# Kernel optimization log

Measured on AMD Instinct MI355X. Metric: run time of the kernel, lower is better.

The kernel has to match this reference:

```python
import jax, jax.numpy as jnp
import numpy as np

LN_EPS = 1e-5


def setup_inputs() -> dict:
    key = jax.random.key(0)
    k1, k2, k3, k4 = jax.random.split(key, 4)
    b, n, d, o, m = 64, 196, 768, 196, 2
    return {
        "x": jax.random.normal(k1, (b, n, d), dtype=jnp.float32),
        "ln_w": jnp.ones((d,), dtype=jnp.float32),
        "ln_b": jnp.zeros((d,), dtype=jnp.float32),
        "sw": jax.random.normal(k2, (o, m, n), dtype=jnp.float32),
        "sb": jax.random.normal(k3, (o, m, n), dtype=jnp.float32),
        "dw": jax.random.normal(k4, (o, m), dtype=jnp.float32),
    }


def reference(x, ln_w, ln_b, sw, sb, dw):
    # LayerNorm over last dim (dim=768)
    mu = jnp.mean(x, axis=-1, keepdims=True)
    var = jnp.mean(jnp.square(x - mu), axis=-1, keepdims=True)
    y = (x - mu) * jax.lax.rsqrt(var + LN_EPS) * ln_w + ln_b  # (b, n, d)

    # Original: repeat y to (b,d,o,m,n), apply sw*y+sb, sum over n.
    # With no synapse activation / dropout this is exactly a contraction:
    # s[b,d,o,m] = sum_n sw[o,m,n]*y[b,n,d] + sum_n sb[o,m,n]
    s = jnp.einsum('bnd,omn->bdom', y, sw) + jnp.sum(sb, axis=-1)  # (b,d,o,m)

    # dendritic weighting then sum over branches m
    t = jnp.sum(dw * s, axis=-1)  # (b, d, o)

    # soma = nn.GELU (exact erf form)
    out = jax.nn.gelu(t, approximate=False)

    out = jnp.transpose(out, (0, 2, 1))  # (b, o, d) == (b, n, d)
    return x * (out + 1.0)
```

## Files before the change

kernel.cpp:

```cpp
#include <hip/hip_runtime.h>
#include <math.h>


#define B_   64
#define N_   196
#define D_   768
#define KP   256

typedef __attribute__((ext_vector_type(8))) short bf16x8;
typedef __attribute__((ext_vector_type(4))) float f32x4;

__device__ __forceinline__ unsigned short bf16_rne(float f) {
    unsigned u = __builtin_bit_cast(unsigned, f);
    u += 0x7FFFu + ((u >> 16) & 1u);
    return (unsigned short)(u >> 16);
}
__device__ __forceinline__ float bf16_to_f(unsigned short h) {
    unsigned u = ((unsigned)h) << 16;
    return __builtin_bit_cast(float, u);
}

__global__ void prep_w_kernel(const float* __restrict__ sw,
                              const float* __restrict__ sb,
                              const float* __restrict__ dw,
                              unsigned short* __restrict__ Whi,
                              unsigned short* __restrict__ Wlo,
                              float* __restrict__ rowsum,
                              float* __restrict__ cvec) {
    int o = blockIdx.x;
    int t = threadIdx.x;
    float w0 = 0.f, w1 = 0.f;
    if (o < N_) { w0 = dw[o * 2 + 0]; w1 = dw[o * 2 + 1]; }
    float val = 0.f, sbp = 0.f;
    if (o < N_ && t < N_) {
        val = w0 * sw[(o * 2 + 0) * N_ + t] + w1 * sw[(o * 2 + 1) * N_ + t];
        sbp = w0 * sb[(o * 2 + 0) * N_ + t] + w1 * sb[(o * 2 + 1) * N_ + t];
    }
    unsigned short h = bf16_rne(val);
    Whi[o * KP + t] = h;
    Wlo[o * KP + t] = bf16_rne(val - bf16_to_f(h));
    __shared__ float r1[256], r2[256];
    r1[t] = val; r2[t] = sbp;
    __syncthreads();
    for (int s = 128; s > 0; s >>= 1) {
        if (t < s) { r1[t] += r1[t + s]; r2[t] += r2[t + s]; }
        __syncthreads();
    }
    if (t == 0) { rowsum[o] = r1[0]; cvec[o] = r2[0]; }
}

__global__ void ln_stats_kernel(const float* __restrict__ x,
                                float* __restrict__ mu,
                                float* __restrict__ rstd) {
    int wave = threadIdx.x >> 6;
    int lane = threadIdx.x & 63;
    int row  = blockIdx.x * 4 + wave;
    const float4* xr = reinterpret_cast<const float4*>(x + (size_t)row * D_);
    float4 v0 = xr[lane];
    float4 v1 = xr[lane + 64];
    float4 v2 = xr[lane + 128];
    float s = v0.x + v0.y + v0.z + v0.w
            + v1.x + v1.y + v1.z + v1.w
            + v2.x + v2.y + v2.z + v2.w;
    #pragma unroll
    for (int off = 32; off >= 1; off >>= 1) s += __shfl_xor(s, off);
    float m = s * (1.0f / D_);
    float q = 0.f;
    {
        float d;
        d = v0.x - m; q += d * d;  d = v0.y - m; q += d * d;
        d = v0.z - m; q += d * d;  d = v0.w - m; q += d * d;
        d = v1.x - m; q += d * d;  d = v1.y - m; q += d * d;
        d = v1.z - m; q += d * d;  d = v1.w - m; q += d * d;
        d = v2.x - m; q += d * d;  d = v2.y - m; q += d * d;
        d = v2.z - m; q += d * d;  d = v2.w - m; q += d * d;
    }
    #pragma unroll
    for (int off = 32; off >= 1; off >>= 1) q += __shfl_xor(q, off);
    if (lane == 0) {
        mu[row]   = m;
        rstd[row] = rsqrtf(q * (1.0f / D_) + 1e-5f);
    }
}

__global__ __launch_bounds__(512, 4) void gemm_mfma_kernel(
    const float* __restrict__ x,
    const float* __restrict__ ln_w,
    const float* __restrict__ ln_b,
    const unsigned short* __restrict__ Whi,
    const unsigned short* __restrict__ Wlo,
    const float* __restrict__ rowsum,
    const float* __restrict__ cvec,
    const float* __restrict__ mu,
    const float* __restrict__ rstd,
    float* __restrict__ out) {
    const int b  = blockIdx.y;
    const int d0 = blockIdx.x * 64;
    const int t = threadIdx.x;
    const int w = t >> 6, lane = t & 63;
    const int m16 = lane & 15, g = lane >> 4;

    __shared__ __align__(16) unsigned short BsH[32 * 64 * 8];
    __shared__ __align__(16) unsigned short BsL[32 * 64 * 8];

    const float* xb  = x + (size_t)b * (N_ * D_);
    const float* mub = mu + b * N_;
    const float* rsb = rstd + b * N_;

    float xv[4][8];
    #pragma unroll
    for (int p = 0; p < 4; ++p) {
        const int koct = p * 8 + w;
        #pragma unroll
        for (int e = 0; e < 8; ++e) {
            const int k = koct * 8 + e;
            xv[p][e] = (k < N_) ? xb[(size_t)k * D_ + d0 + lane] : 0.f;
        }
    }
    #pragma unroll
    for (int p = 0; p < 4; ++p) {
        const int koct = p * 8 + w;
        bf16x8 hv, lv;
        #pragma unroll
        for (int e = 0; e < 8; ++e) {
            const int k = koct * 8 + e;
            float v = 0.f;
            if (k < N_) v = (xv[p][e] - mub[k]) * rsb[k];
            unsigned short h = bf16_rne(v);
            hv[e] = (short)h;
            lv[e] = (short)bf16_rne(v - bf16_to_f(h));
        }
        const int addr = (koct * 64 + lane) * 8;
        *reinterpret_cast<bf16x8*>(&BsH[addr]) = hv;
        *reinterpret_cast<bf16x8*>(&BsL[addr]) = lv;
    }
    __syncthreads();

    f32x4 acc[2][4];
    #pragma unroll
    for (int i = 0; i < 2; ++i)
        #pragma unroll
        for (int j = 0; j < 4; ++j)
            acc[i][j] = (f32x4){0.f, 0.f, 0.f, 0.f};

    const int arow0 = (w * 32 + 0 * 16 + m16) * KP;
    const int arow1 = (w * 32 + 1 * 16 + m16) * KP;

    bf16x8 ah[2][2], al[2][2];
    ah[0][0] = *reinterpret_cast<const bf16x8*>(&Whi[arow0 + g * 8]);
    ah[0][1] = *reinterpret_cast<const bf16x8*>(&Whi[arow1 + g * 8]);
    al[0][0] = *reinterpret_cast<const bf16x8*>(&Wlo[arow0 + g * 8]);
    al[0][1] = *reinterpret_cast<const bf16x8*>(&Wlo[arow1 + g * 8]);

    #pragma unroll
    for (int kq = 0; kq < 7; ++kq) {
        const int cur = kq & 1, nxt = cur ^ 1;
        if (kq < 6) {
            const int col = (kq + 1) * 32 + g * 8;
            ah[nxt][0] = *reinterpret_cast<const bf16x8*>(&Whi[arow0 + col]);
            ah[nxt][1] = *reinterpret_cast<const bf16x8*>(&Whi[arow1 + col]);
            al[nxt][0] = *reinterpret_cast<const bf16x8*>(&Wlo[arow0 + col]);
            al[nxt][1] = *reinterpret_cast<const bf16x8*>(&Wlo[arow1 + col]);
        }
        #pragma unroll
        for (int nf = 0; nf < 4; ++nf) {
            const int baddr = ((kq * 4 + g) * 64 + nf * 16 + m16) * 8;
            bf16x8 bh = *reinterpret_cast<const bf16x8*>(&BsH[baddr]);
            bf16x8 bl = *reinterpret_cast<const bf16x8*>(&BsL[baddr]);
            #pragma unroll
            for (int mf = 0; mf < 2; ++mf) {
                acc[mf][nf] = __builtin_amdgcn_mfma_f32_16x16x32_bf16(ah[cur][mf], bh, acc[mf][nf], 0, 0, 0);
                acc[mf][nf] = __builtin_amdgcn_mfma_f32_16x16x32_bf16(ah[cur][mf], bl, acc[mf][nf], 0, 0, 0);
                acc[mf][nf] = __builtin_amdgcn_mfma_f32_16x16x32_bf16(al[cur][mf], bh, acc[mf][nf], 0, 0, 0);
            }
        }
    }

    float lwv[4], lbv[4];
    #pragma unroll
    for (int nf = 0; nf < 4; ++nf) {
        lwv[nf] = ln_w[d0 + nf * 16 + m16];
        lbv[nf] = ln_b[d0 + nf * 16 + m16];
    }
    #pragma unroll
    for (int mf = 0; mf < 2; ++mf) {
        #pragma unroll
        for (int r = 0; r < 4; ++r) {
            const int o = w * 32 + mf * 16 + g * 4 + r;
            if (o < N_) {
                const float rs = rowsum[o], cc = cvec[o];
                #pragma unroll
                for (int nf = 0; nf < 4; ++nf) {
                    const int d = d0 + nf * 16 + m16;
                    float T = fmaf(lwv[nf], acc[mf][nf][r], fmaf(lbv[nf], rs, cc));
                    float gl = 0.5f * T * (1.0f + erff(T * 0.70710678118654752f));
                    out[((size_t)(b * N_ + o)) * D_ + d] = xb[(size_t)o * D_ + d] * (gl + 1.0f);
                }
            }
        }
    }
}

extern "C" void kernel_launch(void* const* d_in, const int* in_sizes, int n_in,
                              void* d_out, int out_size, void* d_ws, size_t ws_size,
                              hipStream_t stream) {
    const float* x    = (const float*)d_in[0];
    const float* ln_w = (const float*)d_in[1];
    const float* ln_b = (const float*)d_in[2];
    const float* sw   = (const float*)d_in[3];
    const float* sb   = (const float*)d_in[4];
    const float* dw   = (const float*)d_in[5];
    float* out = (float*)d_out;

    float* wsf = (float*)d_ws;
    float* mu     = wsf;
    float* rstd   = mu + B_ * N_;
    float* rowsum = rstd + B_ * N_;
    float* cvec   = rowsum + KP;
    unsigned short* Whi = (unsigned short*)(cvec + KP);
    unsigned short* Wlo = Whi + KP * KP;

    prep_w_kernel<<<KP, 256, 0, stream>>>(sw, sb, dw, Whi, Wlo, rowsum, cvec);
    ln_stats_kernel<<<(B_ * N_) / 4, 256, 0, stream>>>(x, mu, rstd);
    gemm_mfma_kernel<<<dim3(12, B_), 512, 0, stream>>>(
        x, ln_w, ln_b, Whi, Wlo, rowsum, cvec, mu, rstd, out);
}
```

Baseline: 68.50 us.

## Double-buffer normalized-x tiles in LDS with 1024-thread blocks and swizzle

The GEMM block grows to 16 waves, each owning one 16-row M fragment instead of two. The normalized, split-bf16 x tile is now staged in four 64-row K chunks through a double-buffered LDS ring, so global loads of the next chunk overlap the MFMAs on the current one. An XOR swizzle is applied to the LDS addresses to cut bank conflicts. The cost is extra __syncthreads per chunk, and the per-thread register budget is tighter under launch_bounds(1024, 8).

```diff
diff --git a/kernel.cpp b/kernel.cpp
--- a/kernel.cpp
+++ b/kernel.cpp
@@ -83,7 +83,7 @@
     }
 }
 
-__global__ __launch_bounds__(512, 4) void gemm_mfma_kernel(
+__global__ __launch_bounds__(1024, 8) void gemm_mfma_kernel(
     const float* __restrict__ x,
     const float* __restrict__ ln_w,
     const float* __restrict__ ln_b,
@@ -100,80 +100,87 @@
     const int w = t >> 6, lane = t & 63;
     const int m16 = lane & 15, g = lane >> 4;
 
-    __shared__ __align__(16) unsigned short BsH[32 * 64 * 8];
-    __shared__ __align__(16) unsigned short BsL[32 * 64 * 8];
+    __shared__ __align__(16) unsigned short BsH[2][4096];
+    __shared__ __align__(16) unsigned short BsL[2][4096];
 
     const float* xb  = x + (size_t)b * (N_ * D_);
     const float* mub = mu + b * N_;
     const float* rsb = rstd + b * N_;
 
-    float xv[4][8];
-    #pragma unroll
-    for (int p = 0; p < 4; ++p) {
-        const int koct = p * 8 + w;
+    float xv[4];
+    float mus[4], rss[4];
+
+    auto stage_load = [&](int c) {
         #pragma unroll
-        for (int e = 0; e < 8; ++e) {
-            const int k = koct * 8 + e;
-            xv[p][e] = (k < N_) ? xb[(size_t)k * D_ + d0 + lane] : 0.f;
-        }
-    }
-    #pragma unroll
-    for (int p = 0; p < 4; ++p) {
-        const int koct = p * 8 + w;
-        bf16x8 hv, lv;
+        for (int e = 0; e < 4; ++e) {
+            const int k = c * 64 + w * 4 + e;
+            if (k < N_) {
+                xv[e]  = xb[(size_t)k * D_ + d0 + lane];
+                mus[e] = mub[k];
+                rss[e] = rsb[k];
+            } else {
+                xv[e] = 0.f; mus[e] = 0.f; rss[e] = 0.f;
+            }
+        }
+    };
+    auto stage_write = [&](int buf, int c) {
+        if (c == 3 && w >= 8) return;
+        const int kl0  = w * 4;
+        const int koct = kl0 >> 3;
+        short4 hv, lv;
+        short* hp = &hv.x; short* lp = &lv.x;
         #pragma unroll
-        for (int e = 0; e < 8; ++e) {
-            const int k = koct * 8 + e;
-            float v = 0.f;
-            if (k < N_) v = (xv[p][e] - mub[k]) * rsb[k];
+        for (int e = 0; e < 4; ++e) {
+            float v = (xv[e] - mus[e]) * rss[e];
             unsigned short h = bf16_rne(v);
-            hv[e] = (short)h;
-            lv[e] = (short)bf16_rne(v - bf16_to_f(h));
-        }
-        const int addr = (koct * 64 + lane) * 8;
-        *reinterpret_cast<bf16x8*>(&BsH[addr]) = hv;
-        *reinterpret_cast<bf16x8*>(&BsL[addr]) = lv;
-    }
+            hp[e] = (short)h;
+            lp[e] = (short)bf16_rne(v - bf16_to_f(h));
+        }
+        const int byte = (((koct * 64 + lane) * 8 + (kl0 & 7)) * 2) ^ ((koct & 3) << 5);
+        *reinterpret_cast<short4*>(reinterpret_cast<char*>(BsH[buf]) + byte) = hv;
+        *reinterpret_cast<short4*>(reinterpret_cast<char*>(BsL[buf]) + byte) = lv;
+    };
+
+    stage_load(0);
+    stage_write(0, 0);
     __syncthreads();
 
-    f32x4 acc[2][4];
-    #pragma unroll
-    for (int i = 0; i < 2; ++i)
-        #pragma unroll
-        for (int j = 0; j < 4; ++j)
-            acc[i][j] = (f32x4){0.f, 0.f, 0.f, 0.f};
-
-    const int arow0 = (w * 32 + 0 * 16 + m16) * KP;
-    const int arow1 = (w * 32 + 1 * 16 + m16) * KP;
-
-    bf16x8 ah[2][2], al[2][2];
-    ah[0][0] = *reinterpret_cast<const bf16x8*>(&Whi[arow0 + g * 8]);
-    ah[0][1] = *reinterpret_cast<const bf16x8*>(&Whi[arow1 + g * 8]);
-    al[0][0] = *reinterpret_cast<const bf16x8*>(&Wlo[arow0 + g * 8]);
-    al[0][1] = *reinterpret_cast<const bf16x8*>(&Wlo[arow1 + g * 8]);
+    f32x4 acc[4];
+    #pragma unroll
+    for (int j = 0; j < 4; ++j) acc[j] = (f32x4){0.f, 0.f, 0.f, 0.f};
+
+    const int arow = (w * 16 + m16) * KP;
+    bf16x8 ah, al, ahn, aln;
+    ah = *reinterpret_cast<const bf16x8*>(Whi + arow + g * 8);
+    al = *reinterpret_cast<const bf16x8*>(Wlo + arow + g * 8);
 
     #pragma unroll
     for (int kq = 0; kq < 7; ++kq) {
-        const int cur = kq & 1, nxt = cur ^ 1;
+        const int c = kq >> 1, buf = c & 1;
         if (kq < 6) {
             const int col = (kq + 1) * 32 + g * 8;
-            ah[nxt][0] = *reinterpret_cast<const bf16x8*>(&Whi[arow0 + col]);
-            ah[nxt][1] = *reinterpret_cast<const bf16x8*>(&Whi[arow1 + col]);
-            al[nxt][0] = *reinterpret_cast<const bf16x8*>(&Wlo[arow0 + col]);
-            al[nxt][1] = *reinterpret_cast<const bf16x8*>(&Wlo[arow1 + col]);
-        }
+            ahn = *reinterpret_cast<const bf16x8*>(Whi + arow + col);
+            aln = *reinterpret_cast<const bf16x8*>(Wlo + arow + col);
+        }
+        if ((kq & 1) == 0 && c < 3) stage_load(c + 1);
         #pragma unroll
         for (int nf = 0; nf < 4; ++nf) {
-            const int baddr = ((kq * 4 + g) * 64 + nf * 16 + m16) * 8;
-            bf16x8 bh = *reinterpret_cast<const bf16x8*>(&BsH[baddr]);
-            bf16x8 bl = *reinterpret_cast<const bf16x8*>(&BsL[baddr]);
-            #pragma unroll
-            for (int mf = 0; mf < 2; ++mf) {
-                acc[mf][nf] = __builtin_amdgcn_mfma_f32_16x16x32_bf16(ah[cur][mf], bh, acc[mf][nf], 0, 0, 0);
-                acc[mf][nf] = __builtin_amdgcn_mfma_f32_16x16x32_bf16(ah[cur][mf], bl, acc[mf][nf], 0, 0, 0);
-                acc[mf][nf] = __builtin_amdgcn_mfma_f32_16x16x32_bf16(al[cur][mf], bh, acc[mf][nf], 0, 0, 0);
-            }
-        }
+            const int koct = (kq & 1) * 4 + g;
+            const int byte = ((koct * 64 + nf * 16 + m16) * 16) ^ ((koct & 3) << 5);
+            bf16x8 bh = *reinterpret_cast<const bf16x8*>(
+                reinterpret_cast<const char*>(BsH[buf]) + byte);
+            bf16x8 bl = *reinterpret_cast<const bf16x8*>(
+                reinterpret_cast<const char*>(BsL[buf]) + byte);
+            acc[nf] = __builtin_amdgcn_mfma_f32_16x16x32_bf16(ah, bh, acc[nf], 0, 0, 0);
+            acc[nf] = __builtin_amdgcn_mfma_f32_16x16x32_bf16(ah, bl, acc[nf], 0, 0, 0);
+            acc[nf] = __builtin_amdgcn_mfma_f32_16x16x32_bf16(al, bh, acc[nf], 0, 0, 0);
+        }
+        if ((kq & 1) == 1 && c < 3) {
+            __syncthreads();
+            stage_write((c + 1) & 1, c + 1);
+            __syncthreads();
+        }
+        ah = ahn; al = aln;
     }
 
     float lwv[4], lbv[4];
@@ -183,19 +190,16 @@
         lbv[nf] = ln_b[d0 + nf * 16 + m16];
     }
     #pragma unroll
-    for (int mf = 0; mf < 2; ++mf) {
-        #pragma unroll
-        for (int r = 0; r < 4; ++r) {
-            const int o = w * 32 + mf * 16 + g * 4 + r;
-            if (o < N_) {
-                const float rs = rowsum[o], cc = cvec[o];
-                #pragma unroll
-                for (int nf = 0; nf < 4; ++nf) {
-                    const int d = d0 + nf * 16 + m16;
-                    float T = fmaf(lwv[nf], acc[mf][nf][r], fmaf(lbv[nf], rs, cc));
-                    float gl = 0.5f * T * (1.0f + erff(T * 0.70710678118654752f));
-                    out[((size_t)(b * N_ + o)) * D_ + d] = xb[(size_t)o * D_ + d] * (gl + 1.0f);
-                }
+    for (int r = 0; r < 4; ++r) {
+        const int o = w * 16 + g * 4 + r;
+        if (o < N_) {
+            const float rs = rowsum[o], cc = cvec[o];
+            #pragma unroll
+            for (int nf = 0; nf < 4; ++nf) {
+                const int d = d0 + nf * 16 + m16;
+                float T = fmaf(lwv[nf], acc[nf][r], fmaf(lbv[nf], rs, cc));
+                float gl = 0.5f * T * (1.0f + erff(T * 0.70710678118654752f));
+                out[((size_t)(b * N_ + o)) * D_ + d] = xb[(size_t)o * D_ + d] * (gl + 1.0f);
             }
         }
     }
@@ -222,6 +226,6 @@
 
     prep_w_kernel<<<KP, 256, 0, stream>>>(sw, sb, dw, Whi, Wlo, rowsum, cvec);
     ln_stats_kernel<<<(B_ * N_) / 4, 256, 0, stream>>>(x, mu, rstd);
-    gemm_mfma_kernel<<<dim3(12, B_), 512, 0, stream>>>(
+    gemm_mfma_kernel<<<dim3(12, B_), 1024, 0, stream>>>(
         x, ln_w, ln_b, Whi, Wlo, rowsum, cvec, mu, rstd, out);
 }
```

Measured after the change: 72.92 us. 1.06x slower.

## Pipeline B-tile staging over K chunks and pre-swizzle W into fragment layout

Applied to the files above, without the earlier changes.

Before, the GEMM kernel loaded and normalized all of x into a large LDS buffer up front and only then ran the MFMA loop. Now it streams 32-row K chunks through a double-buffered LDS tile, so global loads for later chunks overlap with MFMAs on the current one. The weight matrix is also pre-swizzled into per-fragment order, so each lane's A load is one contiguous 16-byte read. This shrinks LDS use, which may raise occupancy, at the cost of a __syncthreads per chunk.

```diff
diff --git a/kernel.cpp b/kernel.cpp
--- a/kernel.cpp
+++ b/kernel.cpp
@@ -5,7 +5,8 @@
 #define B_   64
 #define N_   196
 #define D_   768
-#define KP   256
+#define KQ   7
+#define OPAD 256
 
 typedef __attribute__((ext_vector_type(8))) short bf16x8;
 typedef __attribute__((ext_vector_type(4))) float f32x4;
@@ -23,8 +24,8 @@
 __global__ void prep_w_kernel(const float* __restrict__ sw,
                               const float* __restrict__ sb,
                               const float* __restrict__ dw,
-                              unsigned short* __restrict__ Whi,
-                              unsigned short* __restrict__ Wlo,
+                              unsigned short* __restrict__ Wfh,
+                              unsigned short* __restrict__ Wfl,
                               float* __restrict__ rowsum,
                               float* __restrict__ cvec) {
     int o = blockIdx.x;
@@ -36,9 +37,12 @@
         val = w0 * sw[(o * 2 + 0) * N_ + t] + w1 * sw[(o * 2 + 1) * N_ + t];
         sbp = w0 * sb[(o * 2 + 0) * N_ + t] + w1 * sb[(o * 2 + 1) * N_ + t];
     }
-    unsigned short h = bf16_rne(val);
-    Whi[o * KP + t] = h;
-    Wlo[o * KP + t] = bf16_rne(val - bf16_to_f(h));
+    if (t < KQ * 32) {
+        unsigned short h = bf16_rne(val);
+        int addr = ((((o >> 4) * KQ + (t >> 5)) * 4 + ((t >> 3) & 3)) * 16 + (o & 15)) * 8 + (t & 7);
+        Wfh[addr] = h;
+        Wfl[addr] = bf16_rne(val - bf16_to_f(h));
+    }
     __shared__ float r1[256], r2[256];
     r1[t] = val; r2[t] = sbp;
     __syncthreads();
@@ -83,12 +87,45 @@
     }
 }
 
+
+#define LOADC(s, c) do {                                                      \
+    _Pragma("unroll")                                                         \
+    for (int e = 0; e < 4; ++e) {                                             \
+        const int k = (c) * 32 + w * 4 + e;                                   \
+        if (k < N_) {                                                         \
+            xv[s][e]  = xb[(size_t)k * D_ + d0 + lane];                       \
+            mus[s][e] = mub[k];                                               \
+            rss[s][e] = rsb[k];                                               \
+        } else { xv[s][e] = 0.f; mus[s][e] = 0.f; rss[s][e] = 0.f; }          \
+    } } while (0)
+
+#define WRITEC(s) do {                                                        \
+    short4 hv, lv; short* hp = &hv.x; short* lp = &lv.x;                      \
+    _Pragma("unroll")                                                         \
+    for (int e = 0; e < 4; ++e) {                                             \
+        float v = (xv[s][e] - mus[s][e]) * rss[s][e];                         \
+        unsigned short h = bf16_rne(v);                                       \
+        hp[e] = (short)h;                                                     \
+        lp[e] = (short)bf16_rne(v - bf16_to_f(h));                            \
+    }                                                                         \
+    const int ea = ((w >> 1) * 64 + lane) * 8 + (w & 1) * 4;                  \
+    *reinterpret_cast<short4*>(&BsH[s][ea]) = hv;                             \
+    *reinterpret_cast<short4*>(&BsL[s][ea]) = lv; } while (0)
+
+#define LOADA(slot, c) do {                                                   \
+    _Pragma("unroll")                                                         \
+    for (int mf = 0; mf < 2; ++mf) {                                          \
+        const size_t ab = ((size_t)((w * 2 + mf) * KQ + (c)) * 512) + lane * 8;\
+        ah[slot][mf] = *reinterpret_cast<const bf16x8*>(Wfh + ab);            \
+        al[slot][mf] = *reinterpret_cast<const bf16x8*>(Wfl + ab);            \
+    } } while (0)
+
 __global__ __launch_bounds__(512, 4) void gemm_mfma_kernel(
     const float* __restrict__ x,
     const float* __restrict__ ln_w,
     const float* __restrict__ ln_b,
-    const unsigned short* __restrict__ Whi,
-    const unsigned short* __restrict__ Wlo,
+    const unsigned short* __restrict__ Wfh,
+    const unsigned short* __restrict__ Wfl,
     const float* __restrict__ rowsum,
     const float* __restrict__ cvec,
     const float* __restrict__ mu,
@@ -100,41 +137,15 @@
     const int w = t >> 6, lane = t & 63;
     const int m16 = lane & 15, g = lane >> 4;
 
-    __shared__ __align__(16) unsigned short BsH[32 * 64 * 8];
-    __shared__ __align__(16) unsigned short BsL[32 * 64 * 8];
+    __shared__ __align__(16) unsigned short BsH[2][2048];
+    __shared__ __align__(16) unsigned short BsL[2][2048];
 
     const float* xb  = x + (size_t)b * (N_ * D_);
     const float* mub = mu + b * N_;
     const float* rsb = rstd + b * N_;
 
-    float xv[4][8];
-    #pragma unroll
-    for (int p = 0; p < 4; ++p) {
-        const int koct = p * 8 + w;
-        #pragma unroll
-        for (int e = 0; e < 8; ++e) {
-            const int k = koct * 8 + e;
-            xv[p][e] = (k < N_) ? xb[(size_t)k * D_ + d0 + lane] : 0.f;
-        }
-    }
-    #pragma unroll
-    for (int p = 0; p < 4; ++p) {
-        const int koct = p * 8 + w;
-        bf16x8 hv, lv;
-        #pragma unroll
-        for (int e = 0; e < 8; ++e) {
-            const int k = koct * 8 + e;
-            float v = 0.f;
-            if (k < N_) v = (xv[p][e] - mub[k]) * rsb[k];
-            unsigned short h = bf16_rne(v);
-            hv[e] = (short)h;
-            lv[e] = (short)bf16_rne(v - bf16_to_f(h));
-        }
-        const int addr = (koct * 64 + lane) * 8;
-        *reinterpret_cast<bf16x8*>(&BsH[addr]) = hv;
-        *reinterpret_cast<bf16x8*>(&BsL[addr]) = lv;
-    }
-    __syncthreads();
+    float xv[2][4], mus[2][4], rss[2][4];
+    bf16x8 ah[2][2], al[2][2];
 
     f32x4 acc[2][4];
     #pragma unroll
@@ -143,35 +154,31 @@
         for (int j = 0; j < 4; ++j)
             acc[i][j] = (f32x4){0.f, 0.f, 0.f, 0.f};
 
-    const int arow0 = (w * 32 + 0 * 16 + m16) * KP;
-    const int arow1 = (w * 32 + 1 * 16 + m16) * KP;
-
-    bf16x8 ah[2][2], al[2][2];
-    ah[0][0] = *reinterpret_cast<const bf16x8*>(&Whi[arow0 + g * 8]);
-    ah[0][1] = *reinterpret_cast<const bf16x8*>(&Whi[arow1 + g * 8]);
-    al[0][0] = *reinterpret_cast<const bf16x8*>(&Wlo[arow0 + g * 8]);
-    al[0][1] = *reinterpret_cast<const bf16x8*>(&Wlo[arow1 + g * 8]);
-
-    #pragma unroll
-    for (int kq = 0; kq < 7; ++kq) {
-        const int cur = kq & 1, nxt = cur ^ 1;
-        if (kq < 6) {
-            const int col = (kq + 1) * 32 + g * 8;
-            ah[nxt][0] = *reinterpret_cast<const bf16x8*>(&Whi[arow0 + col]);
-            ah[nxt][1] = *reinterpret_cast<const bf16x8*>(&Whi[arow1 + col]);
-            al[nxt][0] = *reinterpret_cast<const bf16x8*>(&Wlo[arow0 + col]);
-            al[nxt][1] = *reinterpret_cast<const bf16x8*>(&Wlo[arow1 + col]);
+    LOADC(0, 0);
+    LOADC(1, 1);
+    LOADA(0, 0);
+    WRITEC(0);
+    __syncthreads();
+
+    #pragma unroll
+    for (int c = 0; c < KQ; ++c) {
+        const int s = c & 1;
+        if (c > 0) {
+            WRITEC(s);
+            __syncthreads();
         }
+        if (c + 2 < KQ) LOADC(s, c + 2);
+        if (c + 1 < KQ) LOADA((c + 1) & 1, c + 1);
         #pragma unroll
         for (int nf = 0; nf < 4; ++nf) {
-            const int baddr = ((kq * 4 + g) * 64 + nf * 16 + m16) * 8;
-            bf16x8 bh = *reinterpret_cast<const bf16x8*>(&BsH[baddr]);
-            bf16x8 bl = *reinterpret_cast<const bf16x8*>(&BsL[baddr]);
+            const int ba = (g * 64 + nf * 16 + m16) * 8;
+            bf16x8 bh = *reinterpret_cast<const bf16x8*>(&BsH[s][ba]);
+            bf16x8 bl = *reinterpret_cast<const bf16x8*>(&BsL[s][ba]);
             #pragma unroll
             for (int mf = 0; mf < 2; ++mf) {
-                acc[mf][nf] = __builtin_amdgcn_mfma_f32_16x16x32_bf16(ah[cur][mf], bh, acc[mf][nf], 0, 0, 0);
-                acc[mf][nf] = __builtin_amdgcn_mfma_f32_16x16x32_bf16(ah[cur][mf], bl, acc[mf][nf], 0, 0, 0);
-                acc[mf][nf] = __builtin_amdgcn_mfma_f32_16x16x32_bf16(al[cur][mf], bh, acc[mf][nf], 0, 0, 0);
+                acc[mf][nf] = __builtin_amdgcn_mfma_f32_16x16x32_bf16(ah[s][mf], bh, acc[mf][nf], 0, 0, 0);
+                acc[mf][nf] = __builtin_amdgcn_mfma_f32_16x16x32_bf16(ah[s][mf], bl, acc[mf][nf], 0, 0, 0);
+                acc[mf][nf] = __builtin_amdgcn_mfma_f32_16x16x32_bf16(al[s][mf], bh, acc[mf][nf], 0, 0, 0);
             }
         }
     }
@@ -216,12 +223,12 @@
     float* mu     = wsf;
     float* rstd   = mu + B_ * N_;
     float* rowsum = rstd + B_ * N_;
-    float* cvec   = rowsum + KP;
-    unsigned short* Whi = (unsigned short*)(cvec + KP);
-    unsigned short* Wlo = Whi + KP * KP;
-
-    prep_w_kernel<<<KP, 256, 0, stream>>>(sw, sb, dw, Whi, Wlo, rowsum, cvec);
+    float* cvec   = rowsum + OPAD;
+    unsigned short* Wfh = (unsigned short*)(cvec + OPAD);
+    unsigned short* Wfl = Wfh + OPAD * (KQ * 32);
+
+    prep_w_kernel<<<OPAD, 256, 0, stream>>>(sw, sb, dw, Wfh, Wfl, rowsum, cvec);
     ln_stats_kernel<<<(B_ * N_) / 4, 256, 0, stream>>>(x, mu, rstd);
     gemm_mfma_kernel<<<dim3(12, B_), 512, 0, stream>>>(
-        x, ln_w, ln_b, Whi, Wlo, rowsum, cvec, mu, rstd, out);
-}
+        x, ln_w, ln_b, Wfh, Wfl, rowsum, cvec, mu, rstd, out);
+}
```

After: 54.82 us. 1.25x faster.
